# Optimization experiments

Measured on AMD Instinct MI355X. Metric: run time of the kernel, lower is better.

## Reference

```python
import jax, jax.numpy as jnp
import numpy as np

WINDOW = 5
D_CONV = 4
HEADDIM = 64
NGROUPS = 1
EPS = 1e-5


def _silu(x):
    return x * jax.nn.sigmoid(x)


def _causal_dwconv(x, w, b):
    # x: (B, L, C), w: (C, K), b: (C,) -- depthwise causal conv along L
    K = w.shape[1]
    L = x.shape[1]
    xp = jnp.pad(x, ((0, 0), (K - 1, 0), (0, 0)))
    y = b
    for k in range(K):
        y = y + xp[:, k:k + L, :] * w[:, k]
    return y


def _mamba2_layer(x, in_w, cw, cb, dtb, A_log, Dh, nw, ow):
    # x: (B, L, dim). Mamba2 mixer (mamba_ssm defaults: ngroups=1, rmsnorm gated, no proj bias)
    B, L, _ = x.shape
    d_inner = nw.shape[0]
    nheads = dtb.shape[0]
    p = d_inner // nheads
    conv_dim = cw.shape[0]
    n = (conv_dim - d_inner) // 2  # d_state
    zxbcdt = x @ in_w.T  # (B, L, 2*d_inner + 2*n + nheads)
    z, xBC, dt = jnp.split(zxbcdt, [d_inner, d_inner + conv_dim], axis=-1)
    dt = jax.nn.softplus(dt + dtb)  # (B, L, h)
    xBC = _silu(_causal_dwconv(xBC, cw, cb))
    xh, Bm, Cm = jnp.split(xBC, [d_inner, d_inner + n], axis=-1)
    xh = xh.reshape(B, L, nheads, p)
    A = -jnp.exp(A_log)  # (h,)

    def step(h, inp):
        dt_t, x_t, B_t, C_t = inp  # (B,h), (B,h,p), (B,n), (B,n)
        decay = jnp.exp(dt_t * A)  # (B,h)
        h = h * decay[..., None, None] + (dt_t[..., None] * x_t)[..., None] * B_t[:, None, None, :]
        y = jnp.einsum('bhpn,bn->bhp', h, C_t)
        return h, y

    h0 = jnp.zeros((B, nheads, p, n), x.dtype)
    _, ys = jax.lax.scan(step, h0, (dt.transpose(1, 0, 2), xh.transpose(1, 0, 2, 3),
                                    Bm.transpose(1, 0, 2), Cm.transpose(1, 0, 2)))
    y = ys.transpose(1, 0, 2, 3) + Dh[None, None, :, None] * xh  # (B, L, h, p)
    y = y.reshape(B, L, d_inner)
    # gated RMSNorm (norm_before_gate=False): gate then normalize
    y = y * _silu(z)
    y = y * jax.lax.rsqrt(jnp.mean(y * y, axis=-1, keepdims=True) + EPS) * nw
    return y @ ow.T


def setup_inputs() -> dict:
    key = jax.random.key(0)
    ks = iter(jax.random.split(key, 24))
    B, T, C = 8, 2048, 3
    dim, depth, d_state, expand = 128, 4, 64, 2
    d_inner = expand * dim
    nheads = d_inner // HEADDIM
    conv_dim = d_inner + 2 * NGROUPS * d_state
    d_in_proj = 2 * d_inner + 2 * NGROUPS * d_state + nheads
    nrm = lambda shp, s=1.0: jax.random.normal(next(ks), shp, jnp.float32) * s
    return {
        'x': nrm((B, T, C)),
        'mlp_w1': nrm((128, C * WINDOW), 0.2), 'mlp_b1': jnp.zeros((128,), jnp.float32),
        'mlp_w2': nrm((dim, 128), 0.1), 'mlp_b2': jnp.zeros((dim,), jnp.float32),
        'cls_token': nrm((1, 1, dim)),
        'in_proj_w': nrm((depth, d_in_proj, dim), 0.05),
        'conv_w': nrm((depth, conv_dim, D_CONV), 0.3),
        'conv_b': jnp.zeros((depth, conv_dim), jnp.float32),
        'dt_bias': nrm((depth, nheads), 0.5),
        'A_log': jnp.log(jax.random.uniform(next(ks), (depth, nheads), jnp.float32, 1.0, 16.0)),
        'Dh': jnp.ones((depth, nheads), jnp.float32),
        'norm_w': jnp.ones((depth, d_inner), jnp.float32),
        'out_proj_w': nrm((depth, dim, d_inner), 0.05),
        'ln_w': jnp.ones((dim,), jnp.float32), 'ln_b': jnp.zeros((dim,), jnp.float32),
        'head_w': nrm((1, dim), 0.1), 'head_b': jnp.zeros((1,), jnp.float32),
    }


def reference(x, mlp_w1, mlp_b1, mlp_w2, mlp_b2, cls_token, in_proj_w, conv_w, conv_b,
              dt_bias, A_log, Dh, norm_w, out_proj_w, ln_w, ln_b, head_w, head_b):
    B, T, C = x.shape
    L = T - WINDOW + 1
    # Unfold + rearrange 'b (c w) l -> b l (w c)' == sliding windows flattened (window outer, channel inner)
    tok = jnp.stack([x[:, k:k + L, :] for k in range(WINDOW)], axis=2).reshape(B, L, WINDOW * C)
    h = jax.nn.gelu(tok @ mlp_w1.T + mlp_b1, approximate=False) @ mlp_w2.T + mlp_b2
    dim = h.shape[-1]
    h = jnp.concatenate([h, jnp.broadcast_to(cls_token, (B, 1, dim))], axis=1)
    for i in range(in_proj_w.shape[0]):
        h = _mamba2_layer(h, in_proj_w[i], conv_w[i], conv_b[i], dt_bias[i],
                          A_log[i], Dh[i], norm_w[i], out_proj_w[i])
    cls = h[:, -1]
    mu = jnp.mean(cls, axis=-1, keepdims=True)
    var = jnp.mean((cls - mu) ** 2, axis=-1, keepdims=True)
    cls_n = (cls - mu) * jax.lax.rsqrt(var + 1e-5) * ln_w + ln_b
    out = (cls_n @ head_w.T + head_b)[:, 0]
    return out, h
```

## Files before the change

### kernel.cpp

```cpp
#include <hip/hip_runtime.h>
#include <math.h>

#define BATCH 8
#define TSEQ 2048
#define CIN 3
#define WIN 5
#define LSEQ 2044
#define LH 2045
#define LHP 2048
#define DIM 128
#define DEPTH 4
#define DIN 256
#define NH 4
#define PDIM 64
#define NSTATE 64
#define CONVD 384
#define DPROJ 644
#define NJT 41
#define QC 64
#define NCH 32
#define LDS2 68
#define LDSY 268
#define LDSH 140
#define FTR 32
#define OTOK 32

typedef __attribute__((ext_vector_type(8))) short bf16x8;
typedef __attribute__((ext_vector_type(4))) float f32x4;
union Frag8 { bf16x8 v; uint2 u[2]; };

__device__ __forceinline__ float sigmoidf_(float x){ return 1.f/(1.f+__expf(-x)); }
__device__ __forceinline__ float siluf_(float x){ return x*sigmoidf_(x); }
__device__ __forceinline__ unsigned short f2bf(float f){
  unsigned int u = __float_as_uint(f);
  return (unsigned short)((u + 0x7FFFu + ((u >> 16) & 1u)) >> 16);
}
__device__ __forceinline__ float bf2f(unsigned short u){
  return __uint_as_float(((unsigned int)u) << 16);
}
__device__ __forceinline__ unsigned int pack2(float a, float b){
  return (unsigned int)f2bf(a) | ((unsigned int)f2bf(b) << 16);
}
__device__ __forceinline__ unsigned int pack2lo(float a, float b){
  float ra = a - bf2f(f2bf(a)), rb = b - bf2f(f2bf(b));
  return (unsigned int)f2bf(ra) | ((unsigned int)f2bf(rb) << 16);
}
__device__ __forceinline__ bf16x8 ldfrag(const unsigned short* base, int off){
  Frag8 f;
  f.u[0] = *(const uint2*)(base + off);
  f.u[1] = *(const uint2*)(base + off + 4);
  return f.v;
}

__global__ void __launch_bounds__(256) k_cast_all(
    const float* __restrict__ w, const float* __restrict__ ow,
    unsigned short* __restrict__ wH, unsigned short* __restrict__ wL,
    unsigned short* __restrict__ oH, unsigned short* __restrict__ oL) {
  int blk = blockIdx.x;
  if (blk < 164) {
    int gid = blk*256 + threadIdx.x;
    int lane = gid & 63;
    int kb = (gid >> 6) & 3;
    int jt = (gid >> 8) % NJT;
    int ly = gid / (NJT*4*64);
    int m = lane & 15, q = lane >> 4;
    int j = jt*16 + m;
    int k = kb*32 + q*8;
    unsigned short hi[8], lo[8];
    if (j < DPROJ) {
      const float* src = w + ((size_t)ly*DPROJ + j)*DIM + k;
#pragma unroll
      for (int i = 0; i < 8; ++i) {
        float v = src[i];
        hi[i] = f2bf(v);
        lo[i] = f2bf(v - bf2f(hi[i]));
      }
    } else {
#pragma unroll
      for (int i = 0; i < 8; ++i) { hi[i] = 0; lo[i] = 0; }
    }
    size_t dst = (size_t)gid*8;
    *(uint4*)(wH + dst) = *(const uint4*)hi;
    *(uint4*)(wL + dst) = *(const uint4*)lo;
  } else {
    int gid = (blk - 164)*256 + threadIdx.x;
    int lane = gid & 63;
    int kb = (gid >> 6) & 7;
    int jt = (gid >> 9) & 7;
    int ly = gid >> 12;
    int m = lane & 15, q = lane >> 4;
    int j = jt*16 + m;
    int k = kb*32 + q*8;
    const float* src = ow + ((size_t)ly*DIM + j)*DIN + k;
    unsigned short hi[8], lo[8];
#pragma unroll
    for (int i = 0; i < 8; ++i) {
      float v = src[i];
      hi[i] = f2bf(v);
      lo[i] = f2bf(v - bf2f(hi[i]));
    }
    size_t dst = (size_t)gid*8;
    *(uint4*)(oH + dst) = *(const uint4*)hi;
    *(uint4*)(oL + dst) = *(const uint4*)lo;
  }
}

__global__ void __launch_bounds__(512) k_front_proj(
    const float* __restrict__ x, const float* __restrict__ w1,
    const float* __restrict__ b1, const float* __restrict__ w2,
    const float* __restrict__ b2, const float* __restrict__ cls,
    const unsigned short* __restrict__ wH, const unsigned short* __restrict__ wL,
    const float* __restrict__ dtb, float* __restrict__ zx) {
  int t = threadIdx.x;
  int b = blockIdx.x >> 6;
  int c0 = (blockIdx.x & 63) * FTR;
  __shared__ __align__(16) float pool[108 + 2176 + 4096 + 8192];
  float* xs   = pool;
  float* w1s  = pool + 108;
  float* h1s  = pool + 108 + 2176;
  float* part = pool + 108 + 2176 + 4096;
  unsigned short* hsH = (unsigned short*)pool;
  unsigned short* hsL = hsH + 32*LDSH;
  for (int i = t; i < (FTR+4)*CIN; i += 512) {
    int row = c0 + i/3, ch = i - (i/3)*3;
    xs[i] = (row < TSEQ) ? x[(size_t)b*TSEQ*CIN + (size_t)row*CIN + ch] : 0.f;
  }
  for (int i = t; i < DIM*15; i += 512) {
    int j = i/15, k = i - j*15;
    w1s[j*17+k] = w1[i];
  }
  __syncthreads();
  {
    int j = t & 127, rh = t >> 7;
    float bias = b1[j];
    const float* wr = &w1s[j*17];
    for (int r = rh*8; r < rh*8+8; ++r) {
      float a = bias;
#pragma unroll
      for (int k = 0; k < 15; ++k) a += xs[r*3+k]*wr[k];
      h1s[r*128 + j] = 0.5f*a*(1.f + erff(a*0.70710678118654752f));
    }
  }
  __syncthreads();
  {
    int j = t & 127, z = t >> 7;
    int hf = z & 1, rh2 = z >> 1;
    float4 wv[16];
    const float4* w2r = (const float4*)(w2 + (size_t)j*DIM + hf*64);
#pragma unroll
    for (int k4 = 0; k4 < 16; ++k4) wv[k4] = w2r[k4];
#pragma unroll 2
    for (int r = rh2*16; r < rh2*16+16; ++r) {
      const float4* hr = (const float4*)&h1s[r*128 + hf*64];
      float acc = 0.f;
#pragma unroll
      for (int k4 = 0; k4 < 16; ++k4) {
        float4 hv = hr[k4];
        acc += wv[k4].x*hv.x + wv[k4].y*hv.y + wv[k4].z*hv.z + wv[k4].w*hv.w;
      }
      part[(r*128 + j)*2 + hf] = acc;
    }
  }
  __syncthreads();
  {
    int c = t & 127, rh = t >> 7;
    float bias = b2[c];
    for (int r = rh*8; r < rh*8+8; ++r) {
      int l = c0 + r;
      float val;
      if (l < LSEQ)       val = part[(r*128 + c)*2] + part[(r*128 + c)*2 + 1] + bias;
      else if (l == LSEQ) val = cls[c];
      else                val = 0.f;
      unsigned short hi = f2bf(val);
      hsH[r*LDSH + c] = hi;
      hsL[r*LDSH + c] = f2bf(val - bf2f(hi));
    }
  }
  __syncthreads();
  int wave = t >> 6, lane = t & 63;
  int m = lane & 15, q = lane >> 4;
#pragma unroll 2
  for (int jt = wave; jt < NJT; jt += 8) {
    size_t woff = (((size_t)jt*4)*64 + lane)*8;
    bf16x8 bh[4], bl[4];
#pragma unroll
    for (int kb = 0; kb < 4; ++kb) {
      bh[kb] = *(const bf16x8*)(wH + woff + (size_t)kb*64*8);
      bl[kb] = *(const bf16x8*)(wL + woff + (size_t)kb*64*8);
    }
    f32x4 acc0 = {0.f, 0.f, 0.f, 0.f}, acc1 = {0.f, 0.f, 0.f, 0.f};
#pragma unroll
    for (int kb = 0; kb < 4; ++kb) {
      int o0 = m*LDSH + kb*32 + q*8;
      int o1 = (16 + m)*LDSH + kb*32 + q*8;
      bf16x8 a0h = ldfrag(hsH, o0), a0l = ldfrag(hsL, o0);
      bf16x8 a1h = ldfrag(hsH, o1), a1l = ldfrag(hsL, o1);
      acc0 = __builtin_amdgcn_mfma_f32_16x16x32_bf16(a0l, bh[kb], acc0, 0, 0, 0);
      acc0 = __builtin_amdgcn_mfma_f32_16x16x32_bf16(a0h, bl[kb], acc0, 0, 0, 0);
      acc0 = __builtin_amdgcn_mfma_f32_16x16x32_bf16(a0h, bh[kb], acc0, 0, 0, 0);
      acc1 = __builtin_amdgcn_mfma_f32_16x16x32_bf16(a1l, bh[kb], acc1, 0, 0, 0);
      acc1 = __builtin_amdgcn_mfma_f32_16x16x32_bf16(a1h, bl[kb], acc1, 0, 0, 0);
      acc1 = __builtin_amdgcn_mfma_f32_16x16x32_bf16(a1h, bh[kb], acc1, 0, 0, 0);
    }
    int jj = jt*16 + m;
    if (jj < DPROJ) {
      bool isdt = (jj >= 640);
      float bias = isdt ? dtb[jj - 640] : 0.f;
#pragma unroll
      for (int r = 0; r < 4; ++r) {
        int tok = c0 + q*4 + r;
        if (tok < LH) {
          float vv = acc0[r];
          if (isdt) { vv += bias; vv = (vv > 20.f) ? vv : log1pf(__expf(vv)); }
          zx[((size_t)b*LH + tok)*DPROJ + jj] = vv;
        }
        int tok1 = c0 + 16 + q*4 + r;
        if (tok1 < LH) {
          float vv = acc1[r];
          if (isdt) { vv += bias; vv = (vv > 20.f) ? vv : log1pf(__expf(vv)); }
          zx[((size_t)b*LH + tok1)*DPROJ + jj] = vv;
        }
      }
    }
  }
}

__global__ void k_conv(const float* __restrict__ zx, const float* __restrict__ cw,
                       const float* __restrict__ cb, float* __restrict__ xbc) {
  size_t idx = (size_t)blockIdx.x*blockDim.x + threadIdx.x;
  const size_t total = (size_t)BATCH*LH*(CONVD/4);
  if (idx >= total) return;
  int c4 = (int)(idx % (CONVD/4)) * 4;
  size_t bl = idx / (CONVD/4);
  int l = (int)(bl % LH); int b = (int)(bl / LH);
  float4 w0 = *(const float4*)(cw + (c4+0)*4);
  float4 w1 = *(const float4*)(cw + (c4+1)*4);
  float4 w2 = *(const float4*)(cw + (c4+2)*4);
  float4 w3 = *(const float4*)(cw + (c4+3)*4);
  float4 a = *(const float4*)(cb + c4);
#pragma unroll
  for (int k = 0; k < 4; ++k) {
    int tin = l - 3 + k;
    if (tin >= 0) {
      float4 v = *(const float4*)(zx + ((size_t)b*LH + tin)*DPROJ + DIN + c4);
      a.x += v.x * ((const float*)&w0)[k];
      a.y += v.y * ((const float*)&w1)[k];
      a.z += v.z * ((const float*)&w2)[k];
      a.w += v.w * ((const float*)&w3)[k];
    }
  }
  float4 o;
  o.x = siluf_(a.x); o.y = siluf_(a.y); o.z = siluf_(a.z); o.w = siluf_(a.w);
  *(float4*)(xbc + ((size_t)b*LH + l)*CONVD + c4) = o;
}

__global__ void __launch_bounds__(256, 4) k_chunk_state(
    const float* __restrict__ zx, const float* __restrict__ xbc,
    const float* __restrict__ A_log, float* __restrict__ G, float* __restrict__ dec) {
  int blk = blockIdx.x;
  int c = blk & (NCH-1), hd = (blk >> 5) & 3, b = blk >> 7;
  int t0 = c*QC;
  int tid = threadIdx.x;
  int wv = tid >> 6, lane = tid & 63;
  int m = lane & 15, q = lane >> 4;
  float A = -__expf(A_log[hd]);
  __shared__ __align__(16) unsigned short BcH[QC*LDS2], BcL[QC*LDS2];
  __shared__ __align__(16) unsigned short XtH[QC*LDS2], XtL[QC*LDS2];
  __shared__ float coef[QC];
  float dtv = 0.f;
  if (tid < 64) {
    int tg = t0 + tid;
    dtv = (tg < LH) ? zx[((size_t)b*LH + tg)*DPROJ + 640 + hd] : 0.f;
  }
  float pb[16], px[16];
#pragma unroll
  for (int it = 0; it < 8; ++it) {
    int i = tid + it*256;
    int n = i & 63, s2 = (i >> 6)*2;
    int tg0 = t0 + s2, tg1 = tg0 + 1;
    float b0 = 0.f, b1 = 0.f, x0 = 0.f, x1 = 0.f;
    if (tg0 < LH) {
      size_t row = ((size_t)b*LH + tg0)*CONVD;
      b0 = xbc[row + DIN + n];
      x0 = xbc[row + hd*PDIM + n];
    }
    if (tg1 < LH) {
      size_t row = ((size_t)b*LH + tg1)*CONVD;
      b1 = xbc[row + DIN + n];
      x1 = xbc[row + hd*PDIM + n];
    }
    pb[it*2] = b0; pb[it*2+1] = b1; px[it*2] = x0; px[it*2+1] = x1;
  }
  if (tid < 64) {
    float s = dtv;
#pragma unroll
    for (int off = 1; off < 64; off <<= 1) {
      float u = __shfl_up(s, off);
      if (tid >= off) s += u;
    }
    float cq = __shfl(s, 63);
    coef[tid] = __expf(A*(cq - s)) * dtv;
    if (tid == 63) dec[blk] = __expf(A * s);
  }
  __syncthreads();
#pragma unroll
  for (int it = 0; it < 8; ++it) {
    int i = tid + it*256;
    int n = i & 63, s2 = (i >> 6)*2;
    float c0_ = coef[s2], c1_ = coef[s2+1];
    float b0 = pb[it*2]*c0_, b1 = pb[it*2+1]*c1_;
    float x0 = px[it*2],     x1 = px[it*2+1];
    int o = n*LDS2 + s2;
    *(unsigned int*)(BcH + o) = pack2(b0, b1);
    *(unsigned int*)(BcL + o) = pack2lo(b0, b1);
    *(unsigned int*)(XtH + o) = pack2(x0, x1);
    *(unsigned int*)(XtL + o) = pack2lo(x0, x1);
  }
  __syncthreads();
  bf16x8 ah[2], al[2];
#pragma unroll
  for (int kc = 0; kc < 2; ++kc) {
    int off = (wv*16 + m)*LDS2 + kc*32 + q*8;
    ah[kc] = ldfrag(BcH, off);
    al[kc] = ldfrag(BcL, off);
  }
#pragma unroll
  for (int nt = 0; nt < 4; ++nt) {
    f32x4 acc = {0.f,0.f,0.f,0.f};
#pragma unroll
    for (int kc = 0; kc < 2; ++kc) {
      int off = (nt*16 + m)*LDS2 + kc*32 + q*8;
      bf16x8 xh = ldfrag(XtH, off), xl = ldfrag(XtL, off);
      acc = __builtin_amdgcn_mfma_f32_16x16x32_bf16(al[kc], xh, acc, 0, 0, 0);
      acc = __builtin_amdgcn_mfma_f32_16x16x32_bf16(ah[kc], xl, acc, 0, 0, 0);
      acc = __builtin_amdgcn_mfma_f32_16x16x32_bf16(ah[kc], xh, acc, 0, 0, 0);
    }
    int p = nt*16 + m;
#pragma unroll
    for (int r = 0; r < 4; ++r) {
      int n = wv*16 + q*4 + r;
      G[(size_t)blk*4096 + n*64 + p] = acc[r];
    }
  }
}

__global__ void __launch_bounds__(256) k_combine(
    const float* __restrict__ G, const float* __restrict__ dec, float* __restrict__ Hin) {
  int bh = blockIdx.x >> 2, esp = blockIdx.x & 3;
  int e = esp*1024 + threadIdx.x*4;
  size_t base0 = (size_t)bh*NCH*4096 + e;
  float4 gq[4]; float dq[4];
#pragma unroll
  for (int k = 0; k < 4; ++k) {
    gq[k] = *(const float4*)(G + base0 + (size_t)k*4096);
    dq[k] = dec[bh*NCH + k];
  }
  float4 H = make_float4(0.f,0.f,0.f,0.f);
#pragma unroll 4
  for (int c = 0; c < NCH; ++c) {
    int slot = c & 3;
    float4 g = gq[slot]; float d = dq[slot];
    if (c + 4 < NCH) {
      gq[slot] = *(const float4*)(G + base0 + (size_t)(c+4)*4096);
      dq[slot] = dec[bh*NCH + c + 4];
    }
    *(float4*)(Hin + base0 + (size_t)c*4096) = H;
    H.x = H.x*d + g.x; H.y = H.y*d + g.y; H.z = H.z*d + g.z; H.w = H.w*d + g.w;
  }
}

__global__ void __launch_bounds__(256, 4) k_chunk_out(
    const float* __restrict__ zx, const float* __restrict__ xbc,
    const float* __restrict__ A_log, const float* __restrict__ Hin,
    float* __restrict__ y) {
  int blk = blockIdx.x;
  int c = blk & (NCH-1), hd = (blk >> 5) & 3, b = blk >> 7;
  int t0 = c*QC;
  int tid = threadIdx.x;
  int wv = tid >> 6, lane = tid & 63;
  int m = lane & 15, q = lane >> 4;
  float A = -__expf(A_log[hd]);
  __shared__ __align__(16) unsigned short P0H[QC*LDS2], P0L[QC*LDS2];
  __shared__ __align__(16) unsigned short P1H[QC*LDS2], P1L[QC*LDS2];
  __shared__ float cum[QC], dts[QC], pref[QC];
  float dtv = 0.f;
  if (tid < 64) {
    int tg = t0 + tid;
    dtv = (tg < LH) ? zx[((size_t)b*LH + tg)*DPROJ + 640 + hd] : 0.f;
  }
  float pbv[16], pcv[16];
#pragma unroll
  for (int it = 0; it < 8; ++it) {
    int i = tid + it*256;
    int s = i >> 5, j2 = (i & 31)*2;
    int tg = t0 + s;
    float b0 = 0.f, b1 = 0.f, c0_ = 0.f, c1_ = 0.f;
    if (tg < LH) {
      size_t row = ((size_t)b*LH + tg)*CONVD;
      float2 bv = *(const float2*)(xbc + row + DIN + j2);
      float2 cv = *(const float2*)(xbc + row + DIN + NSTATE + j2);
      b0 = bv.x; b1 = bv.y; c0_ = cv.x; c1_ = cv.y;
    }
    pbv[it*2] = b0; pbv[it*2+1] = b1; pcv[it*2] = c0_; pcv[it*2+1] = c1_;
  }
  size_t hbase = (size_t)blk*4096;
  float hv[16];
#pragma unroll
  for (int it = 0; it < 8; ++it) {
    int i = tid + it*256;
    int p = i & 63, n2 = (i >> 6)*2;
    hv[it*2]   = Hin[hbase + (size_t)n2*64 + p];
    hv[it*2+1] = Hin[hbase + (size_t)(n2+1)*64 + p];
  }
  if (tid < 64) {
    float s = dtv;
#pragma unroll
    for (int off = 1; off < 64; off <<= 1) {
      float u = __shfl_up(s, off);
      if (tid >= off) s += u;
    }
    dts[tid] = dtv; cum[tid] = s; pref[tid] = __expf(A*s);
  }
#pragma unroll
  for (int it = 0; it < 8; ++it) {
    int i = tid + it*256;
    int s = i >> 5, j2 = (i & 31)*2;
    int o = s*LDS2 + j2;
    *(unsigned int*)(P1H + o) = pack2(pbv[it*2], pbv[it*2+1]);
    *(unsigned int*)(P1L + o) = pack2lo(pbv[it*2], pbv[it*2+1]);
    *(unsigned int*)(P0H + o) = pack2(pcv[it*2], pcv[it*2+1]);
    *(unsigned int*)(P0L + o) = pack2lo(pcv[it*2], pcv[it*2+1]);
  }
  __syncthreads();
  bf16x8 ch[2], cl[2];
#pragma unroll
  for (int kc = 0; kc < 2; ++kc) {
    int off = (wv*16 + m)*LDS2 + kc*32 + q*8;
    ch[kc] = ldfrag(P0H, off);
    cl[kc] = ldfrag(P0L, off);
  }
  f32x4 sacc[4];
#pragma unroll
  for (int nt = 0; nt < 4; ++nt) {
    f32x4 a1 = {0.f,0.f,0.f,0.f};
#pragma unroll
    for (int kc = 0; kc < 2; ++kc) {
      int off = (nt*16 + m)*LDS2 + kc*32 + q*8;
      bf16x8 bh = ldfrag(P1H, off), bl = ldfrag(P1L, off);
      a1 = __builtin_amdgcn_mfma_f32_16x16x32_bf16(cl[kc], bh, a1, 0, 0, 0);
      a1 = __builtin_amdgcn_mfma_f32_16x16x32_bf16(ch[kc], bl, a1, 0, 0, 0);
      a1 = __builtin_amdgcn_mfma_f32_16x16x32_bf16(ch[kc], bh, a1, 0, 0, 0);
    }
    sacc[nt] = a1;
  }
  __syncthreads();
  float xv[16];
#pragma unroll
  for (int it = 0; it < 8; ++it) {
    int i = tid + it*256;
    int p = i & 63, s2 = (i >> 6)*2;
    int tg = t0 + s2;
    xv[it*2]   = (tg < LH)   ? xbc[((size_t)b*LH + tg)*CONVD + hd*PDIM + p]   : 0.f;
    xv[it*2+1] = (tg+1 < LH) ? xbc[((size_t)b*LH + tg+1)*CONVD + hd*PDIM + p] : 0.f;
  }
#pragma unroll
  for (int nt = 0; nt < 4; ++nt) {
    int s = nt*16 + m;
#pragma unroll
    for (int r = 0; r < 4; ++r) {
      int t = wv*16 + q*4 + r;
      float mv = 0.f;
      if (s <= t) mv = sacc[nt][r] * __expf(A*(cum[t] - cum[s])) * dts[s];
      unsigned short hi = f2bf(mv);
      P0H[t*LDS2 + s] = hi;
      P0L[t*LDS2 + s] = f2bf(mv - bf2f(hi));
    }
  }
#pragma unroll
  for (int it = 0; it < 8; ++it) {
    int i = tid + it*256;
    int p = i & 63, n2 = (i >> 6)*2;
    int o = p*LDS2 + n2;
    *(unsigned int*)(P1H + o) = pack2(hv[it*2], hv[it*2+1]);
    *(unsigned int*)(P1L + o) = pack2lo(hv[it*2], hv[it*2+1]);
  }
  __syncthreads();
  f32x4 y2a[4];
#pragma unroll
  for (int nt = 0; nt < 4; ++nt) {
    f32x4 a2 = {0.f,0.f,0.f,0.f};
#pragma unroll
    for (int kc = 0; kc < 2; ++kc) {
      int off = (nt*16 + m)*LDS2 + kc*32 + q*8;
      bf16x8 th = ldfrag(P1H, off), tl = ldfrag(P1L, off);
      a2 = __builtin_amdgcn_mfma_f32_16x16x32_bf16(cl[kc], th, a2, 0, 0, 0);
      a2 = __builtin_amdgcn_mfma_f32_16x16x32_bf16(ch[kc], tl, a2, 0, 0, 0);
      a2 = __builtin_amdgcn_mfma_f32_16x16x32_bf16(ch[kc], th, a2, 0, 0, 0);
    }
    y2a[nt] = a2;
  }
  bf16x8 mh[2], ml[2];
#pragma unroll
  for (int kc = 0; kc < 2; ++kc) {
    int off = (wv*16 + m)*LDS2 + kc*32 + q*8;
    mh[kc] = ldfrag(P0H, off);
    ml[kc] = ldfrag(P0L, off);
  }
  __syncthreads();
#pragma unroll
  for (int it = 0; it < 8; ++it) {
    int i = tid + it*256;
    int p = i & 63, s2 = (i >> 6)*2;
    int o = p*LDS2 + s2;
    *(unsigned int*)(P1H + o) = pack2(xv[it*2], xv[it*2+1]);
    *(unsigned int*)(P1L + o) = pack2lo(xv[it*2], xv[it*2+1]);
  }
  __syncthreads();
#pragma unroll
  for (int nt = 0; nt < 4; ++nt) {
    f32x4 a1 = {0.f,0.f,0.f,0.f};
#pragma unroll
    for (int kc = 0; kc < 2; ++kc) {
      int off = (nt*16 + m)*LDS2 + kc*32 + q*8;
      bf16x8 th = ldfrag(P1H, off), tl = ldfrag(P1L, off);
      a1 = __builtin_amdgcn_mfma_f32_16x16x32_bf16(ml[kc], th, a1, 0, 0, 0);
      a1 = __builtin_amdgcn_mfma_f32_16x16x32_bf16(mh[kc], tl, a1, 0, 0, 0);
      a1 = __builtin_amdgcn_mfma_f32_16x16x32_bf16(mh[kc], th, a1, 0, 0, 0);
    }
    int p = nt*16 + m;
#pragma unroll
    for (int r = 0; r < 4; ++r) {
      int t = wv*16 + q*4 + r, tg = t0 + t;
      if (tg < LH)
        y[((size_t)b*LH + tg)*DIN + hd*PDIM + p] = a1[r] + pref[t]*y2a[nt][r];
    }
  }
}

__global__ void __launch_bounds__(512, 4) k_out_fused(
    const float* __restrict__ y, const float* __restrict__ xbc,
    float* __restrict__ zx, const float* __restrict__ Dh,
    const float* __restrict__ nw, const unsigned short* __restrict__ oH,
    const unsigned short* __restrict__ oL,
    const unsigned short* __restrict__ wH, const unsigned short* __restrict__ wL,
    const float* __restrict__ dtb, float* __restrict__ hout, int doProj) {
  int b = blockIdx.x >> 6;
  int l0 = (blockIdx.x & 63) * OTOK;
  int t = threadIdx.x;
  __shared__ __align__(16) unsigned short yH[OTOK*LDSY], yL[OTOK*LDSY];
  __shared__ __align__(16) unsigned short hsH[OTOK*LDSH], hsL[OTOK*LDSH];
  __shared__ float red[OTOK][4];
  __shared__ float rs[OTOK];
  int wave = t >> 6, lane = t & 63;
  bf16x8 pwh[4], pwl[4];
#pragma unroll
  for (int kb = 0; kb < 4; ++kb) {
    size_t woff = (((size_t)wave*8 + kb)*64 + lane)*8;
    pwh[kb] = *(const bf16x8*)(oH + woff);
    pwl[kb] = *(const bf16x8*)(oL + woff);
  }
  int c = t & 255;
  int rh = t >> 8;
  int r0 = rh*16;
  int hd = c >> 6;
  float dcoef = Dh[hd];
  float nwc = nw[c];
  float v[16];
#pragma unroll
  for (int r = 0; r < 16; ++r) {
    int l = l0 + r0 + r;
    float val = 0.f;
    if (l < LH) {
      size_t row = (size_t)b*LH + l;
      float ys = y[row*DIN + c];
      float xh = xbc[row*CONVD + c];
      float z  = zx[row*DPROJ + c];
      val = (ys + dcoef*xh) * siluf_(z);
    }
    v[r] = val;
  }
  int qw = wave & 3;
#pragma unroll
  for (int r = 0; r < 16; ++r) {
    float sq = v[r]*v[r];
    for (int off = 32; off > 0; off >>= 1) sq += __shfl_down(sq, off);
    if (lane == 0) red[r0 + r][qw] = sq;
  }
  __syncthreads();
  if (t < OTOK) {
    float sm = red[t][0]+red[t][1]+red[t][2]+red[t][3];
    rs[t] = rsqrtf(sm/(float)DIN + 1e-5f);
  }
  __syncthreads();
#pragma unroll
  for (int r = 0; r < 16; ++r) {
    float val = v[r] * rs[r0 + r] * nwc;
    unsigned short hi = f2bf(val);
    yH[(r0 + r)*LDSY + c] = hi;
    yL[(r0 + r)*LDSY + c] = f2bf(val - bf2f(hi));
  }
  __syncthreads();
  int m = lane & 15, q = lane >> 4;
  {
    int jt = wave;
    f32x4 acc0 = {0.f,0.f,0.f,0.f}, acc1 = {0.f,0.f,0.f,0.f};
#pragma unroll
    for (int kb = 0; kb < 8; ++kb) {
      bf16x8 bh, bl;
      if (kb < 4) { bh = pwh[kb]; bl = pwl[kb]; }
      else {
        size_t woff = (((size_t)jt*8 + kb)*64 + lane)*8;
        bh = *(const bf16x8*)(oH + woff);
        bl = *(const bf16x8*)(oL + woff);
      }
      int o0 = m*LDSY + kb*32 + q*8;
      int o1 = (16 + m)*LDSY + kb*32 + q*8;
      bf16x8 a0h = ldfrag(yH, o0), a0l = ldfrag(yL, o0);
      bf16x8 a1h = ldfrag(yH, o1), a1l = ldfrag(yL, o1);
      acc0 = __builtin_amdgcn_mfma_f32_16x16x32_bf16(a0l, bh, acc0, 0, 0, 0);
      acc0 = __builtin_amdgcn_mfma_f32_16x16x32_bf16(a0h, bl, acc0, 0, 0, 0);
      acc0 = __builtin_amdgcn_mfma_f32_16x16x32_bf16(a0h, bh, acc0, 0, 0, 0);
      acc1 = __builtin_amdgcn_mfma_f32_16x16x32_bf16(a1l, bh, acc1, 0, 0, 0);
      acc1 = __builtin_amdgcn_mfma_f32_16x16x32_bf16(a1h, bl, acc1, 0, 0, 0);
      acc1 = __builtin_amdgcn_mfma_f32_16x16x32_bf16(a1h, bh, acc1, 0, 0, 0);
    }
    int j = jt*16 + m;
#pragma unroll
    for (int r = 0; r < 4; ++r) {
      int rr = q*4 + r;
      float val = acc0[r];
      unsigned short hi = f2bf(val);
      hsH[rr*LDSH + j] = hi;
      hsL[rr*LDSH + j] = f2bf(val - bf2f(hi));
      int l = l0 + rr;
      if (!doProj && l < LH) hout[((size_t)b*LH + l)*DIM + j] = val;
      int rr1 = 16 + q*4 + r;
      float val1 = acc1[r];
      unsigned short hi1 = f2bf(val1);
      hsH[rr1*LDSH + j] = hi1;
      hsL[rr1*LDSH + j] = f2bf(val1 - bf2f(hi1));
      int l1 = l0 + rr1;
      if (!doProj && l1 < LH) hout[((size_t)b*LH + l1)*DIM + j] = val1;
    }
  }
  if (!doProj) return;
  __syncthreads();
#pragma unroll 2
  for (int jt = wave; jt < NJT; jt += 8) {
    size_t woff = (((size_t)jt*4)*64 + lane)*8;
    bf16x8 bh[4], bl[4];
#pragma unroll
    for (int kb = 0; kb < 4; ++kb) {
      bh[kb] = *(const bf16x8*)(wH + woff + (size_t)kb*64*8);
      bl[kb] = *(const bf16x8*)(wL + woff + (size_t)kb*64*8);
    }
    f32x4 acc0 = {0.f, 0.f, 0.f, 0.f}, acc1 = {0.f, 0.f, 0.f, 0.f};
#pragma unroll
    for (int kb = 0; kb < 4; ++kb) {
      int o0 = m*LDSH + kb*32 + q*8;
      int o1 = (16 + m)*LDSH + kb*32 + q*8;
      bf16x8 a0h = ldfrag(hsH, o0), a0l = ldfrag(hsL, o0);
      bf16x8 a1h = ldfrag(hsH, o1), a1l = ldfrag(hsL, o1);
      acc0 = __builtin_amdgcn_mfma_f32_16x16x32_bf16(a0l, bh[kb], acc0, 0, 0, 0);
      acc0 = __builtin_amdgcn_mfma_f32_16x16x32_bf16(a0h, bl[kb], acc0, 0, 0, 0);
      acc0 = __builtin_amdgcn_mfma_f32_16x16x32_bf16(a0h, bh[kb], acc0, 0, 0, 0);
      acc1 = __builtin_amdgcn_mfma_f32_16x16x32_bf16(a1l, bh[kb], acc1, 0, 0, 0);
      acc1 = __builtin_amdgcn_mfma_f32_16x16x32_bf16(a1h, bl[kb], acc1, 0, 0, 0);
      acc1 = __builtin_amdgcn_mfma_f32_16x16x32_bf16(a1h, bh[kb], acc1, 0, 0, 0);
    }
    int jj = jt*16 + m;
    if (jj < DPROJ) {
      bool isdt = (jj >= 640);
      float bias = isdt ? dtb[jj - 640] : 0.f;
#pragma unroll
      for (int r = 0; r < 4; ++r) {
        int tok = l0 + q*4 + r;
        if (tok < LH) {
          float vv = acc0[r];
          if (isdt) { vv += bias; vv = (vv > 20.f) ? vv : log1pf(__expf(vv)); }
          zx[((size_t)b*LH + tok)*DPROJ + jj] = vv;
        }
        int tok1 = l0 + 16 + q*4 + r;
        if (tok1 < LH) {
          float vv = acc1[r];
          if (isdt) { vv += bias; vv = (vv > 20.f) ? vv : log1pf(__expf(vv)); }
          zx[((size_t)b*LH + tok1)*DPROJ + jj] = vv;
        }
      }
    }
  }
}

__global__ void k_head(const float* __restrict__ h, const float* __restrict__ lnw,
                       const float* __restrict__ lnb, const float* __restrict__ hw,
                       const float* __restrict__ hb, float* __restrict__ out) {
  int b = blockIdx.x; int t = threadIdx.x;
  __shared__ float red[2];
  int wave = t >> 6, lane = t & 63;
  float v = h[((size_t)b*LH + LSEQ)*DIM + t];
  float s = v;
  for (int off = 32; off > 0; off >>= 1) s += __shfl_down(s, off);
  if (lane == 0) red[wave] = s;
  __syncthreads();
  float mean = (red[0]+red[1]) / (float)DIM;
  __syncthreads();
  float d = v - mean; float sq = d*d;
  for (int off = 32; off > 0; off >>= 1) sq += __shfl_down(sq, off);
  if (lane == 0) red[wave] = sq;
  __syncthreads();
  float var = (red[0]+red[1]) / (float)DIM;
  float cn = d*rsqrtf(var + 1e-5f)*lnw[t] + lnb[t];
  float dot = cn*hw[t];
  __syncthreads();
  for (int off = 32; off > 0; off >>= 1) dot += __shfl_down(dot, off);
  if (lane == 0) red[wave] = dot;
  __syncthreads();
  if (t == 0) out[b] = red[0]+red[1] + hb[0];
}

extern "C" void kernel_launch(void* const* d_in, const int* in_sizes, int n_in,
                              void* d_out, int out_size, void* d_ws, size_t ws_size,
                              hipStream_t stream) {
  const float* x     = (const float*)d_in[0];
  const float* w1    = (const float*)d_in[1];
  const float* b1    = (const float*)d_in[2];
  const float* w2    = (const float*)d_in[3];
  const float* b2    = (const float*)d_in[4];
  const float* cls   = (const float*)d_in[5];
  const float* inw   = (const float*)d_in[6];
  const float* cw    = (const float*)d_in[7];
  const float* cb    = (const float*)d_in[8];
  const float* dtb   = (const float*)d_in[9];
  const float* Alog  = (const float*)d_in[10];
  const float* Dh    = (const float*)d_in[11];
  const float* nw    = (const float*)d_in[12];
  const float* ow    = (const float*)d_in[13];
  const float* lnw   = (const float*)d_in[14];
  const float* lnb   = (const float*)d_in[15];
  const float* hw    = (const float*)d_in[16];
  const float* hb    = (const float*)d_in[17];

  float* ws   = (float*)d_ws;
  float* zx   = ws;
  float* xbc  = zx + (size_t)BATCH*LH*DPROJ;
  float* ybuf = xbc + (size_t)BATCH*LH*CONVD;
  float* G    = ybuf;
  float* Hin  = ybuf + 4194304;
  float* dec  = Hin  + 4194304;
  unsigned short* wH = (unsigned short*)(dec + 1024);
  unsigned short* wL = wH + (size_t)DEPTH*NJT*4*64*8;
  unsigned short* oH = wL + (size_t)DEPTH*NJT*4*64*8;
  unsigned short* oL = oH + (size_t)DEPTH*8*8*64*8;

  float* hout = (float*)d_out + 8;

  k_cast_all<<<228, 256, 0, stream>>>(inw, ow, wH, wL, oH, oL);

  k_front_proj<<<BATCH*64, 512, 0, stream>>>(x, w1, b1, w2, b2, cls,
                                             wH, wL, dtb, zx);

  for (int i = 0; i < DEPTH; ++i) {
    int doProj = (i < DEPTH-1) ? 1 : 0;
    int nxt = doProj ? (i+1) : 0;
    k_conv<<<(int)(((long)BATCH*LH*(CONVD/4) + 255)/256), 256, 0, stream>>>(
        zx, cw + (size_t)i*CONVD*4, cb + (size_t)i*CONVD, xbc);
    k_chunk_state<<<BATCH*NH*NCH, 256, 0, stream>>>(zx, xbc, Alog + i*NH, G, dec);
    k_combine<<<BATCH*NH*4, 256, 0, stream>>>(G, dec, Hin);
    k_chunk_out<<<BATCH*NH*NCH, 256, 0, stream>>>(zx, xbc, Alog + i*NH, Hin, ybuf);
    k_out_fused<<<BATCH*64, 512, 0, stream>>>(
        ybuf, xbc, zx, Dh + i*NH, nw + (size_t)i*DIN,
        oH + (size_t)i*8*8*64*8, oL + (size_t)i*8*8*64*8,
        wH + (size_t)nxt*NJT*4*64*8, wL + (size_t)nxt*NJT*4*64*8,
        dtb + nxt*NH, hout, doProj);
  }

  k_head<<<BATCH, 128, 0, stream>>>(hout, lnw, lnb, hw, hb, (float*)d_out);
}
```

Measured before the change: 474.3 us.

## Fuse chunk-state combine into chunk_state via last-block atomic counter

Removes the separate k_combine launch per layer. Each k_chunk_state block bumps a per-(batch,head) atomic counter after writing its G tile, and the last block to finish runs the sequential inter-chunk scan over all 32 chunks to produce Hin. The counters are zeroed by an extra block in k_cast_all. This saves four launches, but the scan now runs in 32 blocks (one per batch-head) instead of 128, so that tail becomes more serial and is exposed at the end of the kernel.

New measurement: 1.195 ms. 152% more time.

```diff
diff --git a/kernel.cpp b/kernel.cpp
--- a/kernel.cpp
+++ b/kernel.cpp
@@ -7,7 +7,6 @@
 #define WIN 5
 #define LSEQ 2044
 #define LH 2045
-#define LHP 2048
 #define DIM 128
 #define DEPTH 4
 #define DIN 256
@@ -55,7 +54,8 @@
 __global__ void __launch_bounds__(256) k_cast_all(
     const float* __restrict__ w, const float* __restrict__ ow,
     unsigned short* __restrict__ wH, unsigned short* __restrict__ wL,
-    unsigned short* __restrict__ oH, unsigned short* __restrict__ oL) {
+    unsigned short* __restrict__ oH, unsigned short* __restrict__ oL,
+    unsigned int* __restrict__ cnt) {
   int blk = blockIdx.x;
   if (blk < 164) {
     int gid = blk*256 + threadIdx.x;
@@ -82,7 +82,7 @@
     size_t dst = (size_t)gid*8;
     *(uint4*)(wH + dst) = *(const uint4*)hi;
     *(uint4*)(wL + dst) = *(const uint4*)lo;
-  } else {
+  } else if (blk < 228) {
     int gid = (blk - 164)*256 + threadIdx.x;
     int lane = gid & 63;
     int kb = (gid >> 6) & 7;
@@ -102,6 +102,9 @@
     size_t dst = (size_t)gid*8;
     *(uint4*)(oH + dst) = *(const uint4*)hi;
     *(uint4*)(oL + dst) = *(const uint4*)lo;
+  } else {
+    int t = threadIdx.x;
+    if (t < DEPTH*32) cnt[t] = 0u;
   }
 }
 
@@ -256,7 +259,8 @@
 
 __global__ void __launch_bounds__(256, 4) k_chunk_state(
     const float* __restrict__ zx, const float* __restrict__ xbc,
-    const float* __restrict__ A_log, float* __restrict__ G, float* __restrict__ dec) {
+    const float* __restrict__ A_log, float* __restrict__ G, float* __restrict__ dec,
+    float* __restrict__ Hin, unsigned int* __restrict__ cnt) {
   int blk = blockIdx.x;
   int c = blk & (NCH-1), hd = (blk >> 5) & 3, b = blk >> 7;
   int t0 = c*QC;
@@ -267,6 +271,7 @@
   __shared__ __align__(16) unsigned short BcH[QC*LDS2], BcL[QC*LDS2];
   __shared__ __align__(16) unsigned short XtH[QC*LDS2], XtL[QC*LDS2];
   __shared__ float coef[QC];
+  __shared__ unsigned int lastflag;
   float dtv = 0.f;
   if (tid < 64) {
     int tg = t0 + tid;
@@ -342,30 +347,49 @@
       G[(size_t)blk*4096 + n*64 + p] = acc[r];
     }
   }
-}
-
-__global__ void __launch_bounds__(256) k_combine(
-    const float* __restrict__ G, const float* __restrict__ dec, float* __restrict__ Hin) {
-  int bh = blockIdx.x >> 2, esp = blockIdx.x & 3;
-  int e = esp*1024 + threadIdx.x*4;
-  size_t base0 = (size_t)bh*NCH*4096 + e;
-  float4 gq[4]; float dq[4];
-#pragma unroll
-  for (int k = 0; k < 4; ++k) {
-    gq[k] = *(const float4*)(G + base0 + (size_t)k*4096);
-    dq[k] = dec[bh*NCH + k];
-  }
-  float4 H = make_float4(0.f,0.f,0.f,0.f);
+  __threadfence();
+  __syncthreads();
+  if (tid == 0) lastflag = (atomicAdd(&cnt[blk >> 5], 1u) == (unsigned)(NCH - 1));
+  __syncthreads();
+  if (lastflag) {
+    __threadfence();
+    int bh = blk >> 5;
+    size_t gbase = (size_t)bh*(size_t)NCH*4096;
+    int e = tid*4;
+    float4 gq0[4], gq1[4], gq2[4], gq3[4]; float dq[4];
+#pragma unroll
+    for (int k = 0; k < 4; ++k) {
+      size_t kb = gbase + (size_t)k*4096 + e;
+      gq0[k] = *(const float4*)(G + kb);
+      gq1[k] = *(const float4*)(G + kb + 1024);
+      gq2[k] = *(const float4*)(G + kb + 2048);
+      gq3[k] = *(const float4*)(G + kb + 3072);
+      dq[k] = dec[bh*NCH + k];
+    }
+    float4 H0 = make_float4(0.f,0.f,0.f,0.f), H1 = H0, H2 = H0, H3 = H0;
 #pragma unroll 4
-  for (int c = 0; c < NCH; ++c) {
-    int slot = c & 3;
-    float4 g = gq[slot]; float d = dq[slot];
-    if (c + 4 < NCH) {
-      gq[slot] = *(const float4*)(G + base0 + (size_t)(c+4)*4096);
-      dq[slot] = dec[bh*NCH + c + 4];
-    }
-    *(float4*)(Hin + base0 + (size_t)c*4096) = H;
-    H.x = H.x*d + g.x; H.y = H.y*d + g.y; H.z = H.z*d + g.z; H.w = H.w*d + g.w;
+    for (int cc = 0; cc < NCH; ++cc) {
+      int slot = cc & 3;
+      float d = dq[slot];
+      float4 g0 = gq0[slot], g1 = gq1[slot], g2 = gq2[slot], g3 = gq3[slot];
+      if (cc + 4 < NCH) {
+        size_t kb = gbase + (size_t)(cc+4)*4096 + e;
+        gq0[slot] = *(const float4*)(G + kb);
+        gq1[slot] = *(const float4*)(G + kb + 1024);
+        gq2[slot] = *(const float4*)(G + kb + 2048);
+        gq3[slot] = *(const float4*)(G + kb + 3072);
+        dq[slot] = dec[bh*NCH + cc + 4];
+      }
+      size_t ob = gbase + (size_t)cc*4096 + e;
+      *(float4*)(Hin + ob)        = H0;
+      *(float4*)(Hin + ob + 1024) = H1;
+      *(float4*)(Hin + ob + 2048) = H2;
+      *(float4*)(Hin + ob + 3072) = H3;
+      H0.x = H0.x*d + g0.x; H0.y = H0.y*d + g0.y; H0.z = H0.z*d + g0.z; H0.w = H0.w*d + g0.w;
+      H1.x = H1.x*d + g1.x; H1.y = H1.y*d + g1.y; H1.z = H1.z*d + g1.z; H1.w = H1.w*d + g1.w;
+      H2.x = H2.x*d + g2.x; H2.y = H2.y*d + g2.y; H2.z = H2.z*d + g2.z; H2.w = H2.w*d + g2.w;
+      H3.x = H3.x*d + g3.x; H3.y = H3.y*d + g3.y; H3.z = H3.z*d + g3.z; H3.w = H3.w*d + g3.w;
+    }
   }
 }
 
@@ -751,10 +775,11 @@
   unsigned short* wL = wH + (size_t)DEPTH*NJT*4*64*8;
   unsigned short* oH = wL + (size_t)DEPTH*NJT*4*64*8;
   unsigned short* oL = oH + (size_t)DEPTH*8*8*64*8;
+  unsigned int*   cnt = (unsigned int*)(oL + (size_t)DEPTH*8*8*64*8);
 
   float* hout = (float*)d_out + 8;
 
-  k_cast_all<<<228, 256, 0, stream>>>(inw, ow, wH, wL, oH, oL);
+  k_cast_all<<<229, 256, 0, stream>>>(inw, ow, wH, wL, oH, oL, cnt);
 
   k_front_proj<<<BATCH*64, 512, 0, stream>>>(x, w1, b1, w2, b2, cls,
                                              wH, wL, dtb, zx);
@@ -764,8 +789,8 @@
     int nxt = doProj ? (i+1) : 0;
     k_conv<<<(int)(((long)BATCH*LH*(CONVD/4) + 255)/256), 256, 0, stream>>>(
         zx, cw + (size_t)i*CONVD*4, cb + (size_t)i*CONVD, xbc);
-    k_chunk_state<<<BATCH*NH*NCH, 256, 0, stream>>>(zx, xbc, Alog + i*NH, G, dec);
-    k_combine<<<BATCH*NH*4, 256, 0, stream>>>(G, dec, Hin);
+    k_chunk_state<<<BATCH*NH*NCH, 256, 0, stream>>>(
+        zx, xbc, Alog + i*NH, G, dec, Hin, cnt + i*32);
     k_chunk_out<<<BATCH*NH*NCH, 256, 0, stream>>>(zx, xbc, Alog + i*NH, Hin, ybuf);
     k_out_fused<<<BATCH*64, 512, 0, stream>>>(
         ybuf, xbc, zx, Dh + i*NH, nw + (size_t)i*DIN,
```
